# Kernel tuning notes

Measured on AMD Instinct MI355X. Metric: run time of the kernel, lower is better.

## Reference

```python
import jax
import jax.numpy as jnp
import numpy as np

# ---- static config (mirrors ReduceMask.__init__ / get_block_params) ----
N, H, W = 32, 1024, 1024
BH, BW = 16, 16            # block_size (pool window)
KH, KW = 3, 3              # kernel_size
SH, SW = 1, 1              # stride
PH, PW = KH // 2, KW // 2  # symmetric padding = 1,1
BSH, BSW = BH - KH + SH, BW - KW + SW   # block_stride = 14,14
BCH = (H + 2 * PH - BH) // BSH + 1      # block_cnt h = 73
BCW = (W + 2 * PW - BW) // BSW + 1      # block_cnt w = 73
THRESHOLD = 0.9
TOTAL = N * BCH * BCW      # fixed upper bound on number of active blocks


def setup_inputs() -> dict:
    key = jax.random.key(0)
    mask = jax.random.uniform(key, (N, 1, H, W), dtype=jnp.float32)
    return {"mask": mask}


def reference(mask):
    # pad H,W by kernel_size//2 (constant zeros), as in F.pad(mask, padding)
    x = jnp.pad(mask, ((0, 0), (0, 0), (PH, PH), (PW, PW)))
    # max_pool2d with window=block_size, stride=block_stride, padding=0
    pooled = jax.lax.reduce_window(
        x, -jnp.inf, jax.lax.max,
        window_dimensions=(1, 1, BH, BW),
        window_strides=(1, 1, BSH, BSW),
        padding='VALID',
    )[:, 0]  # squeeze channel -> [N, BCH, BCW]
    active = pooled > THRESHOLD
    # torch.nonzero -> row-major (n, bh, bw) indices; fixed-size padded with -1 for jit
    nz = jnp.nonzero(active, size=TOTAL, fill_value=-1)
    return jnp.stack(nz, axis=1).astype(jnp.int32)  # [TOTAL, 3]
```

## Files before the change

kernel.cpp:

```cpp
#include <hip/hip_runtime.h>

#define NI    32
#define HH    1024
#define WW    1024
#define BHW   16
#define BS    14
#define NBH   73
#define NBW   73
#define NCHUNK (NI * NBH)
#define TOTAL  (NI * NBH * NBW)

__global__ __launch_bounds__(256) void fill_kernel(int4* __restrict__ out, int n4) {
    int i = blockIdx.x * blockDim.x + threadIdx.x;
    if (i < n4) out[i] = make_int4(-1, -1, -1, -1);
}

__global__ __launch_bounds__(256) void pool_kernel(const float* __restrict__ mask,
                                                   unsigned char* __restrict__ flags,
                                                   int* __restrict__ counts) {
    const int chunk = blockIdx.x;
    const int n  = chunk / NBH;
    const int by = chunk % NBH;
    const int tid = threadIdx.x;

    __shared__ float colmax[WW];
    __shared__ int cnt;
    if (tid == 0) cnt = 0;

    const float* base = mask + (size_t)n * HH * WW;
    const int r0 = by * BS - 1;
    const int c  = tid * 4;

    float4 m = make_float4(-1e30f, -1e30f, -1e30f, -1e30f);
    #pragma unroll
    for (int dr = 0; dr < BHW; ++dr) {
        const int r = r0 + dr;
        if (r >= 0 && r < HH) {
            const float4 v = *(const float4*)(base + (size_t)r * WW + c);
            m.x = fmaxf(m.x, v.x);
            m.y = fmaxf(m.y, v.y);
            m.z = fmaxf(m.z, v.z);
            m.w = fmaxf(m.w, v.w);
        }
    }
    colmax[c + 0] = m.x;
    colmax[c + 1] = m.y;
    colmax[c + 2] = m.z;
    colmax[c + 3] = m.w;
    __syncthreads();

    if (tid < NBW) {
        const int c0 = tid * BS - 1;
        float mx = -1e30f;
        #pragma unroll
        for (int dc = 0; dc < BHW; ++dc) {
            const int cc = c0 + dc;
            if (cc >= 0 && cc < WW) mx = fmaxf(mx, colmax[cc]);
        }
        const unsigned char f = (mx > 0.9f) ? 1 : 0;
        flags[(size_t)chunk * NBW + tid] = f;
        if (f) atomicAdd(&cnt, 1);
    }
    __syncthreads();
    if (tid == 0) counts[chunk] = cnt;
}

__global__ __launch_bounds__(256) void scan_kernel(const int* __restrict__ counts,
                                                   int* __restrict__ offsets) {
    const int tid = threadIdx.x;
    const int SEG = (NCHUNK + 255) / 256;
    __shared__ int ssum[256];

    int local[(NCHUNK + 255) / 256];
    int s = 0;
    const int b0 = tid * SEG;
    #pragma unroll
    for (int i = 0; i < SEG; ++i) {
        const int idx = b0 + i;
        const int v = (idx < NCHUNK) ? counts[idx] : 0;
        local[i] = v;
        s += v;
    }
    ssum[tid] = s;
    __syncthreads();

    for (int off = 1; off < 256; off <<= 1) {
        const int v = (tid >= off) ? ssum[tid - off] : 0;
        __syncthreads();
        ssum[tid] += v;
        __syncthreads();
    }

    int run = (tid == 0) ? 0 : ssum[tid - 1];
    #pragma unroll
    for (int i = 0; i < SEG; ++i) {
        const int idx = b0 + i;
        if (idx < NCHUNK) offsets[idx] = run;
        run += local[i];
    }
}

__global__ __launch_bounds__(128) void scatter_kernel(const unsigned char* __restrict__ flags,
                                                      const int* __restrict__ offsets,
                                                      int* __restrict__ out) {
    const int chunk = blockIdx.x;
    const int n  = chunk / NBH;
    const int by = chunk % NBH;
    const int tid = threadIdx.x;

    __shared__ int sflag[NBW];
    if (tid < NBW) sflag[tid] = flags[(size_t)chunk * NBW + tid];
    __syncthreads();

    if (tid < NBW && sflag[tid]) {
        int p = 0;
        for (int i = 0; i < tid; ++i) p += sflag[i];
        const int pos = offsets[chunk] + p;
        out[3 * pos + 0] = n;
        out[3 * pos + 1] = by;
        out[3 * pos + 2] = tid;
    }
}

extern "C" void kernel_launch(void* const* d_in, const int* in_sizes, int n_in,
                              void* d_out, int out_size, void* d_ws, size_t ws_size,
                              hipStream_t stream) {
    const float* mask = (const float*)d_in[0];
    int* out = (int*)d_out;

    int* counts  = (int*)d_ws;
    int* offsets = counts + NCHUNK;
    unsigned char* flags = (unsigned char*)(offsets + NCHUNK);

    const int n4 = out_size / 4;
    fill_kernel<<<(n4 + 255) / 256, 256, 0, stream>>>((int4*)d_out, n4);
    pool_kernel<<<NCHUNK, 256, 0, stream>>>(mask, flags, counts);
    scan_kernel<<<1, 256, 0, stream>>>(counts, offsets);
    scatter_kernel<<<NCHUNK, 128, 0, stream>>>(flags, offsets, out);
}
```

Baseline: 203.0 us.

## Drop scan kernel, use ballot bitmasks and per-block prefix sums in scatter

Each pool block now records its 73 active flags as two 64-bit wave ballot masks plus a popcount, replacing byte flags and a shared-memory atomic counter. The separate single-block scan kernel is removed. Each scatter block instead sums the counts of all preceding chunks itself and gets in-row positions from masked popcounts. The row-boundary checks in the pool loop become index clamps, which rely on the inputs being non-negative so a duplicated row stands in for zero padding. The change saves a launch and a serial scan stage, at the cost of redundant prefix reads of the counts array in every scatter block.

```diff
diff --git a/kernel.cpp b/kernel.cpp
--- a/kernel.cpp
+++ b/kernel.cpp
@@ -10,13 +10,15 @@
 #define NCHUNK (NI * NBH)
 #define TOTAL  (NI * NBH * NBW)
 
+struct umask2 { unsigned long long x, y; };
+
 __global__ __launch_bounds__(256) void fill_kernel(int4* __restrict__ out, int n4) {
     int i = blockIdx.x * blockDim.x + threadIdx.x;
     if (i < n4) out[i] = make_int4(-1, -1, -1, -1);
 }
 
 __global__ __launch_bounds__(256) void pool_kernel(const float* __restrict__ mask,
-                                                   unsigned char* __restrict__ flags,
+                                                   umask2* __restrict__ masks,
                                                    int* __restrict__ counts) {
     const int chunk = blockIdx.x;
     const int n  = chunk / NBH;
@@ -24,8 +26,7 @@
     const int tid = threadIdx.x;
 
     __shared__ float colmax[WW];
-    __shared__ int cnt;
-    if (tid == 0) cnt = 0;
+    __shared__ unsigned long long sm0, sm1;
 
     const float* base = mask + (size_t)n * HH * WW;
     const int r0 = by * BS - 1;
@@ -34,14 +35,12 @@
     float4 m = make_float4(-1e30f, -1e30f, -1e30f, -1e30f);
     #pragma unroll
     for (int dr = 0; dr < BHW; ++dr) {
-        const int r = r0 + dr;
-        if (r >= 0 && r < HH) {
-            const float4 v = *(const float4*)(base + (size_t)r * WW + c);
-            m.x = fmaxf(m.x, v.x);
-            m.y = fmaxf(m.y, v.y);
-            m.z = fmaxf(m.z, v.z);
-            m.w = fmaxf(m.w, v.w);
-        }
+        const int r = max(r0 + dr, 0);
+        const float4 v = *(const float4*)(base + (size_t)r * WW + c);
+        m.x = fmaxf(m.x, v.x);
+        m.y = fmaxf(m.y, v.y);
+        m.z = fmaxf(m.z, v.z);
+        m.w = fmaxf(m.w, v.w);
     }
     colmax[c + 0] = m.x;
     colmax[c + 1] = m.y;
@@ -49,76 +48,65 @@
     colmax[c + 3] = m.w;
     __syncthreads();
 
+    int f = 0;
     if (tid < NBW) {
         const int c0 = tid * BS - 1;
-        float mx = -1e30f;
+        float mx = colmax[max(c0, 0)];
         #pragma unroll
-        for (int dc = 0; dc < BHW; ++dc) {
-            const int cc = c0 + dc;
-            if (cc >= 0 && cc < WW) mx = fmaxf(mx, colmax[cc]);
-        }
-        const unsigned char f = (mx > 0.9f) ? 1 : 0;
-        flags[(size_t)chunk * NBW + tid] = f;
-        if (f) atomicAdd(&cnt, 1);
+        for (int dc = 1; dc < BHW; ++dc) mx = fmaxf(mx, colmax[c0 + dc]);
+        f = (mx > 0.9f) ? 1 : 0;
     }
+    const unsigned long long b = __ballot(f);
+    const int wave = tid >> 6;
+    const int lane = tid & 63;
+    if (wave == 0 && lane == 0) sm0 = b;
+    if (wave == 1 && lane == 0) sm1 = b;
     __syncthreads();
-    if (tid == 0) counts[chunk] = cnt;
-}
-
-__global__ __launch_bounds__(256) void scan_kernel(const int* __restrict__ counts,
-                                                   int* __restrict__ offsets) {
-    const int tid = threadIdx.x;
-    const int SEG = (NCHUNK + 255) / 256;
-    __shared__ int ssum[256];
-
-    int local[(NCHUNK + 255) / 256];
-    int s = 0;
-    const int b0 = tid * SEG;
-    #pragma unroll
-    for (int i = 0; i < SEG; ++i) {
-        const int idx = b0 + i;
-        const int v = (idx < NCHUNK) ? counts[idx] : 0;
-        local[i] = v;
-        s += v;
-    }
-    ssum[tid] = s;
-    __syncthreads();
-
-    for (int off = 1; off < 256; off <<= 1) {
-        const int v = (tid >= off) ? ssum[tid - off] : 0;
-        __syncthreads();
-        ssum[tid] += v;
-        __syncthreads();
-    }
-
-    int run = (tid == 0) ? 0 : ssum[tid - 1];
-    #pragma unroll
-    for (int i = 0; i < SEG; ++i) {
-        const int idx = b0 + i;
-        if (idx < NCHUNK) offsets[idx] = run;
-        run += local[i];
+    if (tid == 0) {
+        umask2 mm; mm.x = sm0; mm.y = sm1;
+        masks[chunk] = mm;
+        counts[chunk] = __popcll(sm0) + __popcll(sm1);
     }
 }
 
-__global__ __launch_bounds__(128) void scatter_kernel(const unsigned char* __restrict__ flags,
-                                                      const int* __restrict__ offsets,
+__global__ __launch_bounds__(128) void scatter_kernel(const umask2* __restrict__ masks,
+                                                      const int* __restrict__ counts,
                                                       int* __restrict__ out) {
     const int chunk = blockIdx.x;
     const int n  = chunk / NBH;
     const int by = chunk % NBH;
-    const int tid = threadIdx.x;
+    const int tid  = threadIdx.x;
+    const int lane = tid & 63;
+    const int wave = tid >> 6;
 
-    __shared__ int sflag[NBW];
-    if (tid < NBW) sflag[tid] = flags[(size_t)chunk * NBW + tid];
+    __shared__ int wsum[2];
+
+    int partial = 0;
+    for (int i = tid; i < chunk; i += 128) partial += counts[i];
+    #pragma unroll
+    for (int off = 32; off > 0; off >>= 1) partial += __shfl_down(partial, off, 64);
+    if (lane == 0) wsum[wave] = partial;
+
+    const umask2 m = masks[chunk];
     __syncthreads();
+    const int baseoff = wsum[0] + wsum[1];
 
-    if (tid < NBW && sflag[tid]) {
-        int p = 0;
-        for (int i = 0; i < tid; ++i) p += sflag[i];
-        const int pos = offsets[chunk] + p;
-        out[3 * pos + 0] = n;
-        out[3 * pos + 1] = by;
-        out[3 * pos + 2] = tid;
+    if (tid < NBW) {
+        int f, prefix;
+        if (wave == 0) {
+            f = (int)((m.x >> tid) & 1ull);
+            prefix = __popcll(m.x & ((1ull << tid) - 1ull));
+        } else {
+            const int t = tid - 64;
+            f = (int)((m.y >> t) & 1ull);
+            prefix = __popcll(m.x) + __popcll(m.y & ((1ull << t) - 1ull));
+        }
+        if (f) {
+            const int pos = baseoff + prefix;
+            out[3 * pos + 0] = n;
+            out[3 * pos + 1] = by;
+            out[3 * pos + 2] = tid;
+        }
     }
 }
 
@@ -128,13 +116,11 @@
     const float* mask = (const float*)d_in[0];
     int* out = (int*)d_out;
 
-    int* counts  = (int*)d_ws;
-    int* offsets = counts + NCHUNK;
-    unsigned char* flags = (unsigned char*)(offsets + NCHUNK);
+    umask2* masks = (umask2*)d_ws;
+    int* counts = (int*)(masks + NCHUNK);
 
     const int n4 = out_size / 4;
     fill_kernel<<<(n4 + 255) / 256, 256, 0, stream>>>((int4*)d_out, n4);
-    pool_kernel<<<NCHUNK, 256, 0, stream>>>(mask, flags, counts);
-    scan_kernel<<<1, 256, 0, stream>>>(counts, offsets);
-    scatter_kernel<<<NCHUNK, 128, 0, stream>>>(flags, offsets, out);
+    pool_kernel<<<NCHUNK, 256, 0, stream>>>(mask, masks, counts);
+    scatter_kernel<<<NCHUNK, 128, 0, stream>>>(masks, counts, out);
 }
```

New measurement: 193.3 us. 4.8% less time.
